# Performance work log

Measured on AMD Instinct MI355X. Metric: run time of the kernel, lower is better.

Reference implementation:

```python
import jax, jax.numpy as jnp
import numpy as np

N = 4096          # n_nodes
M = 8192          # m_nodes (= 2*N, required by block structure)
D = 128           # in_dim == hidden_dim (conv1 is reapplied to its own output)
H = 128
NUM_ITERS = 3


def setup_inputs() -> dict:
    key = jax.random.key(0)
    ks = jax.random.split(key, 6)
    X = jax.random.normal(ks[0], (N, D), dtype=jnp.float32)
    R = jax.random.uniform(ks[1], (N, N), dtype=jnp.float32)
    A = 0.5 * (R + R.T)  # symmetric, strictly positive connectivity matrix
    # upsample MLP: Linear(n_nodes -> m_nodes - n_nodes), torch weight layout [out, in]
    W_up = jax.random.normal(ks[2], (M - N, N), dtype=jnp.float32) * 0.02
    b_up = jnp.zeros((M - N,), dtype=jnp.float32)
    # GCNConv linear weights stored [in, out]
    W1 = jax.random.normal(ks[3], (D, H), dtype=jnp.float32) * 0.05
    b1 = jnp.zeros((H,), dtype=jnp.float32)
    W2 = jax.random.normal(ks[4], (H, H), dtype=jnp.float32) * 0.05
    b2 = jnp.zeros((H,), dtype=jnp.float32)
    return dict(X=X, A=A, W_up=W_up, b_up=b_up, W1=W1, b1=b1, W2=W2, b2=b2)


def _gcn(Adj, X, W, b):
    # PyG GCNConv on a fully dense, strictly-positive weighted graph:
    # every diagonal entry is nonzero, so add_remaining_self_loops is a no-op and
    # out = D^{-1/2} A D^{-1/2} (X W) + b  exactly.
    deg = Adj.sum(axis=0)                         # [m] column degree
    dinv = jnp.where(deg > 0, jax.lax.rsqrt(deg), 0.0)
    An = Adj * dinv[:, None] * dinv[None, :]      # symmetric normalization
    return An @ (X @ W) + b


def reference(X, A, W_up, b_up, W1, b1, W2, b2):
    # new_nodes = upsample_mlp(X.T).T  -> [M-N, D]
    new_nodes = (X.T @ W_up.T + b_up).T
    Xu = jnp.concatenate([X, new_nodes], axis=0)  # [M, D]
    # block adjacency: [[A, A.T], [A, sigmoid(new @ new.T)]]
    Adj = jnp.block([[A, A.T],
                     [A, jax.nn.sigmoid(new_nodes @ new_nodes.T)]])  # [M, M]
    A_out = Adj
    for _ in range(NUM_ITERS):
        Xu = jax.nn.relu(_gcn(Adj, Xu, W1, b1))
        Adj = jax.nn.sigmoid(Xu @ Xu.T)           # mid-loop adjacency rebuild
        Xu = jax.nn.relu(_gcn(Adj, Xu, W2, b2))
        A_out = jax.nn.sigmoid(Xu @ Xu.T)
        # NOTE: edge_index for the next conv1 is NOT rebuilt from A_out in the
        # original (only after conv1), so Adj carries the mid-loop matrix.
    return A_out
```

## Files before the change

kernel.cpp:

```cpp
#include <hip/hip_runtime.h>
#include <hip/hip_bf16.h>


#define N_NODES 4096
#define M_NODES 8192
#define DIM 128
#define SLICE_ELEMS ((size_t)M_NODES * DIM)

typedef __attribute__((ext_vector_type(4))) float f32x4;
typedef __attribute__((ext_vector_type(8))) short bf16x8;

__device__ __forceinline__ unsigned short f2bf(float f) {
  union { float f; unsigned u; } v; v.f = f;
  unsigned r = v.u + 0x7fffu + ((v.u >> 16) & 1u);
  return (unsigned short)(r >> 16);
}

__device__ __forceinline__ void gld16(unsigned short* lds, const unsigned short* g) {
  __builtin_amdgcn_global_load_lds(
      (const __attribute__((address_space(1))) unsigned int*)g,
      (__attribute__((address_space(3))) unsigned int*)lds, 16, 0, 0);
}

__device__ __forceinline__ float sigmoidf_(float x) { return 1.0f / (1.0f + __expf(-x)); }


__global__ void cast_x_kernel(const float* __restrict__ X, unsigned short* __restrict__ Xu,
                              unsigned short* __restrict__ XT) {
  int idx = blockIdx.x * 256 + threadIdx.x;
  int i = idx >> 7, c = idx & 127;
  unsigned short b = f2bf(X[idx]);
  Xu[idx] = b;
  XT[(size_t)c * N_NODES + i] = b;
}

__global__ void cast_wup_kernel(const float4* __restrict__ W, unsigned short* __restrict__ Wb) {
  int idx4 = blockIdx.x * 256 + threadIdx.x;
  int r = idx4 >> 10, c = (idx4 & 1023) << 2;
  float4 v = W[idx4];
  ushort4 o;
  o.x = f2bf(v.x); o.y = f2bf(v.y); o.z = f2bf(v.z); o.w = f2bf(v.w);
  *(ushort4*)&Wb[((size_t)(r >> 6) * 128 + (c >> 5)) * 2048 + (r & 63) * 32 + (c & 31)] = o;
}

__global__ void cast_wt_kernel(const float* __restrict__ W, unsigned short* __restrict__ WT) {
  int idx = blockIdx.x * 256 + threadIdx.x;
  int k = idx >> 7, c = idx & 127;
  WT[c * DIM + k] = f2bf(W[idx]);
}

__global__ void cast_a_kernel(const float* __restrict__ A, unsigned short* __restrict__ Adj,
                              float* __restrict__ colsumA) {
  int c = blockIdx.x * 256 + threadIdx.x;
  int r0 = blockIdx.y * 128;
  size_t cb = (size_t)(c >> 5) * 2048 + (c & 31);
  float s = 0.f;
  for (int r = 0; r < 128; ++r) {
    int i = r0 + r;
    float a = A[(size_t)i * N_NODES + c];
    unsigned short b = f2bf(a);
    size_t rt = (size_t)(i >> 6) * 256 * 2048 + (size_t)(i & 63) * 32;
    Adj[rt + cb] = b;
    Adj[rt + cb + (size_t)128 * 2048] = b;
    Adj[rt + (size_t)64 * 256 * 2048 + cb] = b;
    s += a;
  }
  atomicAdd(&colsumA[c], s);
}

__global__ void init_deg_kernel(const float* __restrict__ colsumA, float* __restrict__ deg) {
  int i = blockIdx.x * 256 + threadIdx.x;
  deg[i] = (i < N_NODES) ? 2.0f * colsumA[i] : colsumA[i - N_NODES];
}


__global__ __launch_bounds__(256)
void agg_kernel(const unsigned short* __restrict__ At, int kChunksTotal,
                const unsigned short* __restrict__ BT, long ldb,
                float* __restrict__ accBase, int kIters) {
  __shared__ __align__(16) unsigned short lA[2048];
  __shared__ __align__(16) unsigned short lB[4096];
  const int t = threadIdx.x, w = t >> 6, lane = t & 63;
  const int q = lane >> 4, l15 = lane & 15;
  const int sg0 = blockIdx.y * kIters;
  const size_t abase = ((size_t)blockIdx.x * kChunksTotal + sg0) * 2048;
  const size_t bk = (size_t)sg0 * 32;
  const int brow = t >> 2, bchk = t & 3;

  f32x4 acc[8];
#pragma unroll
  for (int b = 0; b < 8; ++b) acc[b] = (f32x4)0.f;

  for (int s = 0; s < kIters; ++s) {
    __syncthreads();
    gld16(&lA[t * 8], &At[abase + (size_t)s * 2048 + t * 8]);
    gld16(&lB[t * 8], &BT[(size_t)brow * ldb + bk + s * 32 + bchk * 8]);
    gld16(&lB[2048 + t * 8], &BT[(size_t)(64 + brow) * ldb + bk + s * 32 + bchk * 8]);
    __syncthreads();
    bf16x8 a0 = *(const bf16x8*)&lA[(w * 16 + l15) * 32 + q * 8];
#pragma unroll
    for (int nt = 0; nt < 8; ++nt) {
      bf16x8 b = *(const bf16x8*)&lB[(nt * 16 + l15) * 32 + q * 8];
      acc[nt] = __builtin_amdgcn_mfma_f32_16x16x32_bf16(a0, b, acc[nt], 0, 0, 0);
    }
  }
  float* ct = accBase + (size_t)blockIdx.y * SLICE_ELEMS + (size_t)blockIdx.x * 8192;
#pragma unroll
  for (int nt = 0; nt < 8; ++nt)
    *(f32x4*)&ct[(w * 8 + nt) * 256 + (q * 16 + l15) * 4] = acc[nt];
}

__global__ void reduce_acc_kernel(const float* __restrict__ acc,
                                  unsigned short* __restrict__ dst,
                                  const float* __restrict__ bias_row,
                                  const float* __restrict__ bias_col,
                                  const float* __restrict__ deg, int mode, int nSlices) {
  int p = blockIdx.x * 256 + threadIdx.x;
  float s = 0.f;
  for (int sp = 0; sp < nSlices; ++sp) s += acc[(size_t)sp * SLICE_ELEMS + p];
  int tile = p >> 13, r = p & 8191;
  int grp = r >> 8, r2 = r & 255;
  int w = grp >> 3, nt = grp & 7;
  int i = r2 & 3, ql = r2 >> 2;
  int row = tile * 64 + w * 16 + (ql >> 4) * 4 + i;
  int col = nt * 16 + (ql & 15);
  float v;
  if (mode == 0) v = s + bias_row[row];
  else {
    float d = deg[row];
    float dv = d > 0.f ? rsqrtf(d) : 0.f;
    v = fmaxf(dv * s + bias_col[col], 0.f);
  }
  dst[(size_t)row * DIM + col] = f2bf(v);
}


template <int MODE>
__global__ __launch_bounds__(256)
void rebuild_kernel(const unsigned short* __restrict__ XA,
                    const unsigned short* __restrict__ XB,
                    void* __restrict__ out, long p1 ,
                    long col0, float* __restrict__ deg) {
  __shared__ __align__(16) unsigned short smem[32768];
  __shared__ float lcol[128];
  unsigned short* lA = smem;
  unsigned short* lB = smem + 16384;
  const int t = threadIdx.x, w = t >> 6, lane = t & 63;
  const int q = lane >> 4, l15 = lane & 15;
  const int i0 = blockIdx.x * 128, j0 = blockIdx.y * 128;
  const int srow = t >> 2, schk = t & 3;
#pragma unroll
  for (int kk = 0; kk < 4; ++kk)
#pragma unroll
    for (int h = 0; h < 2; ++h) {
      gld16(&lA[kk * 4096 + h * 2048 + t * 8],
            &XA[(size_t)(i0 + h * 64 + srow) * DIM + kk * 32 + schk * 8]);
      gld16(&lB[kk * 4096 + h * 2048 + t * 8],
            &XB[(size_t)(j0 + h * 64 + srow) * DIM + kk * 32 + schk * 8]);
    }
  if (MODE == 0 && t < 128) lcol[t] = 0.f;
  __syncthreads();

  f32x4 acc[2][8];
#pragma unroll
  for (int a = 0; a < 2; ++a)
#pragma unroll
    for (int b = 0; b < 8; ++b) acc[a][b] = (f32x4)0.f;

#pragma unroll
  for (int kk = 0; kk < 4; ++kk) {
    bf16x8 a0 = *(const bf16x8*)&lA[kk * 4096 + (w * 32 + l15) * 32 + q * 8];
    bf16x8 a1 = *(const bf16x8*)&lA[kk * 4096 + (w * 32 + 16 + l15) * 32 + q * 8];
#pragma unroll
    for (int nt = 0; nt < 8; ++nt) {
      bf16x8 b = *(const bf16x8*)&lB[kk * 4096 + (nt * 16 + l15) * 32 + q * 8];
      acc[0][nt] = __builtin_amdgcn_mfma_f32_16x16x32_bf16(a0, b, acc[0][nt], 0, 0, 0);
      acc[1][nt] = __builtin_amdgcn_mfma_f32_16x16x32_bf16(a1, b, acc[1][nt], 0, 0, 0);
    }
  }
  __syncthreads();

  if (MODE == 0) {
    unsigned short* lC = smem;
#pragma unroll
    for (int mt = 0; mt < 2; ++mt)
#pragma unroll
      for (int nt = 0; nt < 8; ++nt) {
        float cs = 0.f;
#pragma unroll
        for (int i = 0; i < 4; ++i) {
          float sv = sigmoidf_(acc[mt][nt][i]);
          cs += sv;
          lC[(w * 32 + mt * 16 + q * 4 + i) * 136 + nt * 16 + l15] = f2bf(sv);
        }
        cs += __shfl_xor(cs, 16);
        cs += __shfl_xor(cs, 32);
        if (lane < 16) atomicAdd(&lcol[nt * 16 + lane], cs);
      }
    __syncthreads();
    unsigned short* og = (unsigned short*)out;
    const long rowbase = p1 + i0, colbase = col0 + j0;
    const size_t tb = ((size_t)(rowbase >> 6) * 256 + (colbase >> 5)) * 2048;
#pragma unroll
    for (int cc = 0; cc < 8; ++cc) {
      int ch = t + cc * 256;
      int row = ch >> 4, c16 = ch & 15;
      *(bf16x8*)&og[tb + (size_t)(row >> 6) * 256 * 2048 + (size_t)(c16 >> 2) * 2048 +
                    (row & 63) * 32 + (c16 & 3) * 8] =
          *(const bf16x8*)&lC[row * 136 + c16 * 8];
    }
    if (t < 128) atomicAdd(&deg[colbase + t], lcol[t]);
  } else {
    float* og = (float*)out;
    float* lCf = (float*)smem;
#pragma unroll
    for (int h2 = 0; h2 < 2; ++h2) {
      __syncthreads();
      if ((w >> 1) == h2) {
#pragma unroll
        for (int mt = 0; mt < 2; ++mt)
#pragma unroll
          for (int nt = 0; nt < 8; ++nt)
#pragma unroll
            for (int i = 0; i < 4; ++i)
              lCf[((w & 1) * 32 + mt * 16 + q * 4 + i) * 128 + nt * 16 + l15] =
                  sigmoidf_(acc[mt][nt][i]);
      }
      __syncthreads();
#pragma unroll
      for (int j = 0; j < 8; ++j) {
        int ch = t + j * 256;
        int r64 = ch >> 5, c4 = (ch & 31) * 4;
        *(f32x4*)&og[(size_t)(i0 + h2 * 64 + r64) * p1 + j0 + c4] =
            *(const f32x4*)&lCf[r64 * 128 + c4];
      }
    }
  }
}


__global__ __launch_bounds__(256)
void yz_kernel(const unsigned short* __restrict__ Xu, const unsigned short* __restrict__ WT,
               const float* __restrict__ deg, unsigned short* __restrict__ ZT, int ldz) {
  __shared__ __align__(16) unsigned short smem[32768];
  unsigned short* lA = smem;
  unsigned short* lB = smem + 16384;
  const int t = threadIdx.x, w = t >> 6, lane = t & 63;
  const int q = lane >> 4, l15 = lane & 15;
  const int r0 = blockIdx.x * 128;
  const int srow = t >> 2, schk = t & 3;
#pragma unroll
  for (int kk = 0; kk < 4; ++kk)
#pragma unroll
    for (int h = 0; h < 2; ++h) {
      gld16(&lA[kk * 4096 + h * 2048 + t * 8],
            &Xu[(size_t)(r0 + h * 64 + srow) * DIM + kk * 32 + schk * 8]);
      gld16(&lB[kk * 4096 + h * 2048 + t * 8],
            &WT[(size_t)(h * 64 + srow) * DIM + kk * 32 + schk * 8]);
    }
  __syncthreads();

  f32x4 acc[2][8];
#pragma unroll
  for (int a = 0; a < 2; ++a)
#pragma unroll
    for (int b = 0; b < 8; ++b) acc[a][b] = (f32x4)0.f;

#pragma unroll
  for (int kk = 0; kk < 4; ++kk) {
    bf16x8 a0 = *(const bf16x8*)&lA[kk * 4096 + (w * 32 + l15) * 32 + q * 8];
    bf16x8 a1 = *(const bf16x8*)&lA[kk * 4096 + (w * 32 + 16 + l15) * 32 + q * 8];
#pragma unroll
    for (int nt = 0; nt < 8; ++nt) {
      bf16x8 b = *(const bf16x8*)&lB[kk * 4096 + (nt * 16 + l15) * 32 + q * 8];
      acc[0][nt] = __builtin_amdgcn_mfma_f32_16x16x32_bf16(a0, b, acc[0][nt], 0, 0, 0);
      acc[1][nt] = __builtin_amdgcn_mfma_f32_16x16x32_bf16(a1, b, acc[1][nt], 0, 0, 0);
    }
  }
  float dv[2][4];
#pragma unroll
  for (int mt = 0; mt < 2; ++mt)
#pragma unroll
    for (int i = 0; i < 4; ++i) {
      float d = deg[r0 + w * 32 + mt * 16 + q * 4 + i];
      dv[mt][i] = d > 0.f ? rsqrtf(d) : 0.f;
    }
  __syncthreads();
  unsigned short* lT = smem;
#pragma unroll
  for (int mt = 0; mt < 2; ++mt)
#pragma unroll
    for (int nt = 0; nt < 8; ++nt)
#pragma unroll
      for (int i = 0; i < 4; ++i) {
        int r = w * 32 + mt * 16 + q * 4 + i;
        lT[(nt * 16 + l15) * 136 + r] = f2bf(dv[mt][i] * acc[mt][nt][i]);
      }
  __syncthreads();
#pragma unroll
  for (int cc = 0; cc < 8; ++cc) {
    int ch = t + cc * 256;
    int c = ch >> 4, c16 = ch & 15;
    *(bf16x8*)&ZT[(size_t)c * ldz + r0 + c16 * 8] = *(const bf16x8*)&lT[c * 136 + c16 * 8];
  }
}


extern "C" void kernel_launch(void* const* d_in, const int* in_sizes, int n_in,
                              void* d_out, int out_size, void* d_ws, size_t ws_size,
                              hipStream_t stream) {
  (void)in_sizes; (void)n_in; (void)out_size;
  const float* X   = (const float*)d_in[0];
  const float* A   = (const float*)d_in[1];
  const float* Wup = (const float*)d_in[2];
  const float* bup = (const float*)d_in[3];
  const float* W1  = (const float*)d_in[4];
  const float* b1  = (const float*)d_in[5];
  const float* W2  = (const float*)d_in[6];
  const float* b2  = (const float*)d_in[7];

  const size_t ADJ_BYTES = (size_t)M_NODES * M_NODES * 2;
  char* ws = (char*)d_ws;
  size_t off = 0;
  auto alloc = [&](size_t bytes) {
    char* p = ws + off;
    off += (bytes + 255) & ~(size_t)255;
    return p;
  };
  float*          accb    = (float*)alloc(8 * SLICE_ELEMS * 4);
  unsigned short* Xu      = (unsigned short*)alloc((size_t)M_NODES * DIM * 2);
  unsigned short* ZT      = (unsigned short*)alloc((size_t)DIM * M_NODES * 2);
  unsigned short* XT      = (unsigned short*)alloc((size_t)DIM * N_NODES * 2);
  unsigned short* W1T     = (unsigned short*)alloc(DIM * DIM * 2);
  unsigned short* W2T     = (unsigned short*)alloc(DIM * DIM * 2);
  float*          colsumA = (float*)alloc(N_NODES * 4);
  float*          deg     = (float*)alloc(M_NODES * 4);

  unsigned short* Adj;
  if (ws_size >= off + ADJ_BYTES) Adj = (unsigned short*)(ws + off);
  else                            Adj = (unsigned short*)d_out;
  unsigned short* Wupb = Adj;

  unsigned short* XuNew = Xu + (size_t)N_NODES * DIM;

  hipMemsetAsync(colsumA, 0, N_NODES * 4, stream);
  cast_x_kernel<<<N_NODES * DIM / 256, 256, 0, stream>>>(X, Xu, XT);
  cast_wup_kernel<<<((size_t)N_NODES * N_NODES / 4) / 256, 256, 0, stream>>>(
      (const float4*)Wup, Wupb);
  cast_wt_kernel<<<64, 256, 0, stream>>>(W1, W1T);
  cast_wt_kernel<<<64, 256, 0, stream>>>(W2, W2T);

  agg_kernel<<<dim3(N_NODES / 64, 8), 256, 0, stream>>>(
      Wupb, 128, XT, N_NODES, accb, 16);
  reduce_acc_kernel<<<N_NODES * DIM / 256, 256, 0, stream>>>(
      accb, XuNew, bup, nullptr, nullptr, 0, 8);

  cast_a_kernel<<<dim3(N_NODES / 256, N_NODES / 128), 256, 0, stream>>>(A, Adj, colsumA);
  init_deg_kernel<<<M_NODES / 256, 256, 0, stream>>>(colsumA, deg);
  rebuild_kernel<0><<<dim3(N_NODES / 128, N_NODES / 128), 256, 0, stream>>>(
      XuNew, XuNew, Adj, N_NODES, N_NODES, deg);

  for (int it = 0; it < 3; ++it) {
    yz_kernel<<<M_NODES / 128, 256, 0, stream>>>(Xu, W1T, deg, ZT, M_NODES);
    agg_kernel<<<dim3(M_NODES / 64, 8), 256, 0, stream>>>(
        Adj, 256, ZT, M_NODES, accb, 32);
    reduce_acc_kernel<<<M_NODES * DIM / 256, 256, 0, stream>>>(
        accb, Xu, nullptr, b1, deg, 1, 8);
    hipMemsetAsync(deg, 0, M_NODES * 4, stream);
    rebuild_kernel<0><<<dim3(M_NODES / 128, M_NODES / 128), 256, 0, stream>>>(
        Xu, Xu, Adj, 0, 0, deg);
    yz_kernel<<<M_NODES / 128, 256, 0, stream>>>(Xu, W2T, deg, ZT, M_NODES);
    agg_kernel<<<dim3(M_NODES / 64, 8), 256, 0, stream>>>(
        Adj, 256, ZT, M_NODES, accb, 32);
    reduce_acc_kernel<<<M_NODES * DIM / 256, 256, 0, stream>>>(
        accb, Xu, nullptr, b2, deg, 1, 8);
    if (it == 2)
      rebuild_kernel<1><<<dim3(M_NODES / 128, M_NODES / 128), 256, 0, stream>>>(
          Xu, Xu, d_out, M_NODES, 0, nullptr);
  }
}
```

Measured before the change: 989.6 us.

## Store adjacency and aggregation operands in FP8 and use FP8 MFMA

Converts the adjacency matrix, upsample weights, X transpose and the scaled ZT features from bf16 to FP8 (e4m3) storage and switches the aggregation GEMM to fp8 MFMA instructions with 64-wide K tiles. Split-K partial sums are now written as bf16 instead of fp32. This halves the memory traffic of the bandwidth-bound 8192x8192 adjacency reads and writes and of the split-K buffers. In exchange it loses considerable precision in the adjacency values, activations and partial sums, which risks accuracy-tolerance failures.

```diff
diff --git a/kernel.cpp b/kernel.cpp
--- a/kernel.cpp
+++ b/kernel.cpp
@@ -15,8 +15,20 @@
   unsigned r = v.u + 0x7fffu + ((v.u >> 16) & 1u);
   return (unsigned short)(r >> 16);
 }
-
-__device__ __forceinline__ void gld16(unsigned short* lds, const unsigned short* g) {
+__device__ __forceinline__ float bf2f(unsigned short b) {
+  union { unsigned u; float f; } v; v.u = ((unsigned)b) << 16;
+  return v.f;
+}
+__device__ __forceinline__ unsigned char f2fp8(float a) {
+  return (unsigned char)(__builtin_amdgcn_cvt_pk_fp8_f32(a, a, 0, false) & 0xff);
+}
+__device__ __forceinline__ unsigned f2fp8x4(float a, float b, float c, float d) {
+  int p = __builtin_amdgcn_cvt_pk_fp8_f32(a, b, 0, false);
+  p = __builtin_amdgcn_cvt_pk_fp8_f32(c, d, p, true);
+  return (unsigned)p;
+}
+
+__device__ __forceinline__ void gld16(void* lds, const void* g) {
   __builtin_amdgcn_global_load_lds(
       (const __attribute__((address_space(1))) unsigned int*)g,
       (__attribute__((address_space(3))) unsigned int*)lds, 16, 0, 0);
@@ -26,21 +38,20 @@
 
 
 __global__ void cast_x_kernel(const float* __restrict__ X, unsigned short* __restrict__ Xu,
-                              unsigned short* __restrict__ XT) {
+                              unsigned char* __restrict__ XT) {
   int idx = blockIdx.x * 256 + threadIdx.x;
   int i = idx >> 7, c = idx & 127;
-  unsigned short b = f2bf(X[idx]);
-  Xu[idx] = b;
-  XT[(size_t)c * N_NODES + i] = b;
-}
-
-__global__ void cast_wup_kernel(const float4* __restrict__ W, unsigned short* __restrict__ Wb) {
+  float v = X[idx];
+  Xu[idx] = f2bf(v);
+  XT[(size_t)c * N_NODES + i] = f2fp8(v);
+}
+
+__global__ void cast_wup_kernel(const float4* __restrict__ W, unsigned char* __restrict__ Wb) {
   int idx4 = blockIdx.x * 256 + threadIdx.x;
   int r = idx4 >> 10, c = (idx4 & 1023) << 2;
   float4 v = W[idx4];
-  ushort4 o;
-  o.x = f2bf(v.x); o.y = f2bf(v.y); o.z = f2bf(v.z); o.w = f2bf(v.w);
-  *(ushort4*)&Wb[((size_t)(r >> 6) * 128 + (c >> 5)) * 2048 + (r & 63) * 32 + (c & 31)] = o;
+  unsigned p = f2fp8x4(v.x, v.y, v.z, v.w);
+  *(unsigned*)&Wb[((size_t)(r >> 6) * 64 + (c >> 6)) * 4096 + (r & 63) * 64 + (c & 63)] = p;
 }
 
 __global__ void cast_wt_kernel(const float* __restrict__ W, unsigned short* __restrict__ WT) {
@@ -49,20 +60,20 @@
   WT[c * DIM + k] = f2bf(W[idx]);
 }
 
-__global__ void cast_a_kernel(const float* __restrict__ A, unsigned short* __restrict__ Adj,
+__global__ void cast_a_kernel(const float* __restrict__ A, unsigned char* __restrict__ Adj,
                               float* __restrict__ colsumA) {
   int c = blockIdx.x * 256 + threadIdx.x;
   int r0 = blockIdx.y * 128;
-  size_t cb = (size_t)(c >> 5) * 2048 + (c & 31);
+  size_t cb = (size_t)(c >> 6) * 4096 + (c & 63);
   float s = 0.f;
   for (int r = 0; r < 128; ++r) {
     int i = r0 + r;
     float a = A[(size_t)i * N_NODES + c];
-    unsigned short b = f2bf(a);
-    size_t rt = (size_t)(i >> 6) * 256 * 2048 + (size_t)(i & 63) * 32;
+    unsigned char b = f2fp8(a);
+    size_t rt = (size_t)(i >> 6) * 128 * 4096 + (size_t)(i & 63) * 64;
     Adj[rt + cb] = b;
-    Adj[rt + cb + (size_t)128 * 2048] = b;
-    Adj[rt + (size_t)64 * 256 * 2048 + cb] = b;
+    Adj[rt + cb + (size_t)64 * 4096] = b;
+    Adj[rt + (size_t)64 * 128 * 4096 + cb] = b;
     s += a;
   }
   atomicAdd(&colsumA[c], s);
@@ -75,16 +86,15 @@
 
 
 __global__ __launch_bounds__(256)
-void agg_kernel(const unsigned short* __restrict__ At, int kChunksTotal,
-                const unsigned short* __restrict__ BT, long ldb,
-                float* __restrict__ accBase, int kIters) {
-  __shared__ __align__(16) unsigned short lA[2048];
-  __shared__ __align__(16) unsigned short lB[4096];
+void agg_kernel(const unsigned char* __restrict__ At, int kcTotal,
+                const unsigned char* __restrict__ BT, long ldb,
+                unsigned short* __restrict__ accBase, int kIters) {
+  __shared__ __align__(16) unsigned char lA[4096];
+  __shared__ __align__(16) unsigned char lB[8192];
   const int t = threadIdx.x, w = t >> 6, lane = t & 63;
   const int q = lane >> 4, l15 = lane & 15;
-  const int sg0 = blockIdx.y * kIters;
-  const size_t abase = ((size_t)blockIdx.x * kChunksTotal + sg0) * 2048;
-  const size_t bk = (size_t)sg0 * 32;
+  const size_t abase = ((size_t)blockIdx.x * kcTotal + (size_t)blockIdx.y * kIters) * 4096;
+  const size_t bk = (size_t)blockIdx.y * kIters * 64;
   const int brow = t >> 2, bchk = t & 3;
 
   f32x4 acc[8];
@@ -93,31 +103,38 @@
 
   for (int s = 0; s < kIters; ++s) {
     __syncthreads();
-    gld16(&lA[t * 8], &At[abase + (size_t)s * 2048 + t * 8]);
-    gld16(&lB[t * 8], &BT[(size_t)brow * ldb + bk + s * 32 + bchk * 8]);
-    gld16(&lB[2048 + t * 8], &BT[(size_t)(64 + brow) * ldb + bk + s * 32 + bchk * 8]);
+    gld16(&lA[t * 16], &At[abase + (size_t)s * 4096 + t * 16]);
+    gld16(&lB[t * 16], &BT[(size_t)brow * ldb + bk + s * 64 + bchk * 16]);
+    gld16(&lB[4096 + t * 16], &BT[(size_t)(64 + brow) * ldb + bk + s * 64 + bchk * 16]);
     __syncthreads();
-    bf16x8 a0 = *(const bf16x8*)&lA[(w * 16 + l15) * 32 + q * 8];
+    long long a0 = *(const long long*)&lA[(w * 16 + l15) * 64 + q * 8];
+    long long a1 = *(const long long*)&lA[(w * 16 + l15) * 64 + 32 + q * 8];
 #pragma unroll
     for (int nt = 0; nt < 8; ++nt) {
-      bf16x8 b = *(const bf16x8*)&lB[(nt * 16 + l15) * 32 + q * 8];
-      acc[nt] = __builtin_amdgcn_mfma_f32_16x16x32_bf16(a0, b, acc[nt], 0, 0, 0);
-    }
-  }
-  float* ct = accBase + (size_t)blockIdx.y * SLICE_ELEMS + (size_t)blockIdx.x * 8192;
-#pragma unroll
-  for (int nt = 0; nt < 8; ++nt)
-    *(f32x4*)&ct[(w * 8 + nt) * 256 + (q * 16 + l15) * 4] = acc[nt];
-}
-
-__global__ void reduce_acc_kernel(const float* __restrict__ acc,
+      long long b0 = *(const long long*)&lB[(nt * 16 + l15) * 64 + q * 8];
+      long long b1 = *(const long long*)&lB[(nt * 16 + l15) * 64 + 32 + q * 8];
+      acc[nt] = __builtin_amdgcn_mfma_f32_16x16x32_fp8_fp8(a0, b0, acc[nt], 0, 0, 0);
+      acc[nt] = __builtin_amdgcn_mfma_f32_16x16x32_fp8_fp8(a1, b1, acc[nt], 0, 0, 0);
+    }
+  }
+  unsigned short* ct = accBase + (size_t)blockIdx.y * SLICE_ELEMS + (size_t)blockIdx.x * 8192;
+#pragma unroll
+  for (int nt = 0; nt < 8; ++nt) {
+    ushort4 o;
+    o.x = f2bf(acc[nt][0]); o.y = f2bf(acc[nt][1]);
+    o.z = f2bf(acc[nt][2]); o.w = f2bf(acc[nt][3]);
+    *(ushort4*)&ct[(w * 8 + nt) * 256 + (q * 16 + l15) * 4] = o;
+  }
+}
+
+__global__ void reduce_acc_kernel(const unsigned short* __restrict__ acc,
                                   unsigned short* __restrict__ dst,
                                   const float* __restrict__ bias_row,
                                   const float* __restrict__ bias_col,
                                   const float* __restrict__ deg, int mode, int nSlices) {
   int p = blockIdx.x * 256 + threadIdx.x;
   float s = 0.f;
-  for (int sp = 0; sp < nSlices; ++sp) s += acc[(size_t)sp * SLICE_ELEMS + p];
+  for (int sp = 0; sp < nSlices; ++sp) s += bf2f(acc[(size_t)sp * SLICE_ELEMS + p]);
   int tile = p >> 13, r = p & 8191;
   int grp = r >> 8, r2 = r & 255;
   int w = grp >> 3, nt = grp & 7;
@@ -141,10 +158,10 @@
                     const unsigned short* __restrict__ XB,
                     void* __restrict__ out, long p1 ,
                     long col0, float* __restrict__ deg) {
-  __shared__ __align__(16) unsigned short smem[32768];
+  __shared__ __align__(16) unsigned char smem[32768];
   __shared__ float lcol[128];
-  unsigned short* lA = smem;
-  unsigned short* lB = smem + 16384;
+  unsigned short* lA = (unsigned short*)smem;
+  unsigned short* lB = (unsigned short*)(smem + 16384);
   const int t = threadIdx.x, w = t >> 6, lane = t & 63;
   const int q = lane >> 4, l15 = lane & 15;
   const int i0 = blockIdx.x * 128, j0 = blockIdx.y * 128;
@@ -181,7 +198,7 @@
   __syncthreads();
 
   if (MODE == 0) {
-    unsigned short* lC = smem;
+    unsigned char* lC = smem;
 #pragma unroll
     for (int mt = 0; mt < 2; ++mt)
 #pragma unroll
@@ -191,23 +208,23 @@
         for (int i = 0; i < 4; ++i) {
           float sv = sigmoidf_(acc[mt][nt][i]);
           cs += sv;
-          lC[(w * 32 + mt * 16 + q * 4 + i) * 136 + nt * 16 + l15] = f2bf(sv);
+          lC[(w * 32 + mt * 16 + q * 4 + i) * 136 + nt * 16 + l15] = f2fp8(sv);
         }
         cs += __shfl_xor(cs, 16);
         cs += __shfl_xor(cs, 32);
         if (lane < 16) atomicAdd(&lcol[nt * 16 + lane], cs);
       }
     __syncthreads();
-    unsigned short* og = (unsigned short*)out;
+    unsigned char* og = (unsigned char*)out;
     const long rowbase = p1 + i0, colbase = col0 + j0;
-    const size_t tb = ((size_t)(rowbase >> 6) * 256 + (colbase >> 5)) * 2048;
+    const size_t tb = ((size_t)(rowbase >> 6) * 128 + (colbase >> 6)) * 4096;
 #pragma unroll
     for (int cc = 0; cc < 8; ++cc) {
       int ch = t + cc * 256;
-      int row = ch >> 4, c16 = ch & 15;
-      *(bf16x8*)&og[tb + (size_t)(row >> 6) * 256 * 2048 + (size_t)(c16 >> 2) * 2048 +
-                    (row & 63) * 32 + (c16 & 3) * 8] =
-          *(const bf16x8*)&lC[row * 136 + c16 * 8];
+      int row = ch >> 4, c8 = (ch & 15) * 8;
+      *(long long*)&og[tb + (size_t)(row >> 6) * 128 * 4096 + (size_t)(c8 >> 6) * 4096 +
+                       (row & 63) * 64 + (c8 & 63)] =
+          *(const long long*)&lC[row * 136 + c8];
     }
     if (t < 128) atomicAdd(&deg[colbase + t], lcol[t]);
   } else {
@@ -241,10 +258,10 @@
 
 __global__ __launch_bounds__(256)
 void yz_kernel(const unsigned short* __restrict__ Xu, const unsigned short* __restrict__ WT,
-               const float* __restrict__ deg, unsigned short* __restrict__ ZT, int ldz) {
-  __shared__ __align__(16) unsigned short smem[32768];
-  unsigned short* lA = smem;
-  unsigned short* lB = smem + 16384;
+               const float* __restrict__ deg, unsigned char* __restrict__ ZT, long ldz) {
+  __shared__ __align__(16) unsigned char smem[32768];
+  unsigned short* lA = (unsigned short*)smem;
+  unsigned short* lB = (unsigned short*)(smem + 16384);
   const int t = threadIdx.x, w = t >> 6, lane = t & 63;
   const int q = lane >> 4, l15 = lane & 15;
   const int r0 = blockIdx.x * 128;
@@ -286,7 +303,7 @@
       dv[mt][i] = d > 0.f ? rsqrtf(d) : 0.f;
     }
   __syncthreads();
-  unsigned short* lT = smem;
+  unsigned char* lT = smem;
 #pragma unroll
   for (int mt = 0; mt < 2; ++mt)
 #pragma unroll
@@ -294,14 +311,14 @@
 #pragma unroll
       for (int i = 0; i < 4; ++i) {
         int r = w * 32 + mt * 16 + q * 4 + i;
-        lT[(nt * 16 + l15) * 136 + r] = f2bf(dv[mt][i] * acc[mt][nt][i]);
+        lT[(nt * 16 + l15) * 136 + r] = f2fp8(dv[mt][i] * acc[mt][nt][i]);
       }
   __syncthreads();
 #pragma unroll
   for (int cc = 0; cc < 8; ++cc) {
     int ch = t + cc * 256;
-    int c = ch >> 4, c16 = ch & 15;
-    *(bf16x8*)&ZT[(size_t)c * ldz + r0 + c16 * 8] = *(const bf16x8*)&lT[c * 136 + c16 * 8];
+    int c = ch >> 4, r8 = (ch & 15) * 8;
+    *(long long*)&ZT[(size_t)c * ldz + r0 + r8] = *(const long long*)&lT[c * 136 + r8];
   }
 }
 
@@ -319,7 +336,7 @@
   const float* W2  = (const float*)d_in[6];
   const float* b2  = (const float*)d_in[7];
 
-  const size_t ADJ_BYTES = (size_t)M_NODES * M_NODES * 2;
+  const size_t ADJ_BYTES = (size_t)M_NODES * M_NODES;
   char* ws = (char*)d_ws;
   size_t off = 0;
   auto alloc = [&](size_t bytes) {
@@ -327,19 +344,19 @@
     off += (bytes + 255) & ~(size_t)255;
     return p;
   };
-  float*          accb    = (float*)alloc(8 * SLICE_ELEMS * 4);
+  unsigned short* accb    = (unsigned short*)alloc(8 * SLICE_ELEMS * 2);
   unsigned short* Xu      = (unsigned short*)alloc((size_t)M_NODES * DIM * 2);
-  unsigned short* ZT      = (unsigned short*)alloc((size_t)DIM * M_NODES * 2);
-  unsigned short* XT      = (unsigned short*)alloc((size_t)DIM * N_NODES * 2);
+  unsigned char*  ZT      = (unsigned char*)alloc((size_t)DIM * M_NODES);
+  unsigned char*  XT      = (unsigned char*)alloc((size_t)DIM * N_NODES);
   unsigned short* W1T     = (unsigned short*)alloc(DIM * DIM * 2);
   unsigned short* W2T     = (unsigned short*)alloc(DIM * DIM * 2);
   float*          colsumA = (float*)alloc(N_NODES * 4);
   float*          deg     = (float*)alloc(M_NODES * 4);
 
-  unsigned short* Adj;
-  if (ws_size >= off + ADJ_BYTES) Adj = (unsigned short*)(ws + off);
-  else                            Adj = (unsigned short*)d_out;
-  unsigned short* Wupb = Adj;
+  unsigned char* Adj;
+  if (ws_size >= off + ADJ_BYTES) Adj = (unsigned char*)(ws + off);
+  else                            Adj = (unsigned char*)d_out;
+  unsigned char* Wupb = Adj;
 
   unsigned short* XuNew = Xu + (size_t)N_NODES * DIM;
 
@@ -351,7 +368,7 @@
   cast_wt_kernel<<<64, 256, 0, stream>>>(W2, W2T);
 
   agg_kernel<<<dim3(N_NODES / 64, 8), 256, 0, stream>>>(
-      Wupb, 128, XT, N_NODES, accb, 16);
+      Wupb, 64, XT, N_NODES, accb, 8);
   reduce_acc_kernel<<<N_NODES * DIM / 256, 256, 0, stream>>>(
       accb, XuNew, bup, nullptr, nullptr, 0, 8);
 
@@ -363,7 +380,7 @@
   for (int it = 0; it < 3; ++it) {
     yz_kernel<<<M_NODES / 128, 256, 0, stream>>>(Xu, W1T, deg, ZT, M_NODES);
     agg_kernel<<<dim3(M_NODES / 64, 8), 256, 0, stream>>>(
-        Adj, 256, ZT, M_NODES, accb, 32);
+        Adj, 128, ZT, M_NODES, accb, 16);
     reduce_acc_kernel<<<M_NODES * DIM / 256, 256, 0, stream>>>(
         accb, Xu, nullptr, b1, deg, 1, 8);
     hipMemsetAsync(deg, 0, M_NODES * 4, stream);
@@ -371,7 +388,7 @@
         Xu, Xu, Adj, 0, 0, deg);
     yz_kernel<<<M_NODES / 128, 256, 0, stream>>>(Xu, W2T, deg, ZT, M_NODES);
     agg_kernel<<<dim3(M_NODES / 64, 8), 256, 0, stream>>>(
-        Adj, 256, ZT, M_NODES, accb, 32);
+        Adj, 128, ZT, M_NODES, accb, 16);
     reduce_acc_kernel<<<M_NODES * DIM / 256, 256, 0, stream>>>(
         accb, Xu, nullptr, b2, deg, 1, 8);
     if (it == 2)
```

New measurement: 1.161 ms. 17.3% more time.
